# Kernel tuning notes

Hardware: AMD Instinct MI355X
Metric: run time of the kernel (lower is better)

## Reference

```python
import jax, jax.numpy as jnp
import numpy as np

B, T, C, H = 8, 1024, 768, 12
D = C // H  # head dim = 64

def setup_inputs() -> dict:
    key = jax.random.key(0)
    k0, k1, k2, k3, k4 = jax.random.split(key, 5)
    x = jax.random.normal(k0, (B, T, C), dtype=jnp.float32)
    # flax Dense params: kernel [in, out], bias [out]
    c_attn_kernel = jax.random.normal(k1, (C, 3 * C), dtype=jnp.float32) * (1.0 / np.sqrt(C))
    c_attn_bias = jax.random.normal(k2, (3 * C,), dtype=jnp.float32) * 0.01
    c_proj_kernel = jax.random.normal(k3, (C, C), dtype=jnp.float32) * (1.0 / np.sqrt(C))
    c_proj_bias = jax.random.normal(k4, (C,), dtype=jnp.float32) * 0.01
    return {"x": x, "c_attn_kernel": c_attn_kernel, "c_attn_bias": c_attn_bias,
            "c_proj_kernel": c_proj_kernel, "c_proj_bias": c_proj_bias}

def reference(x, c_attn_kernel, c_attn_bias, c_proj_kernel, c_proj_bias):
    Bc, Tc, Cc = x.shape
    qkv = x @ c_attn_kernel + c_attn_bias          # [B, T, 3C]
    q, k, v = jnp.split(qkv, 3, axis=-1)
    q = q.reshape(Bc, Tc, H, D).swapaxes(1, 2)     # [B, H, T, D]
    k = k.reshape(Bc, Tc, H, D).swapaxes(1, 2)
    v = v.reshape(Bc, Tc, H, D).swapaxes(1, 2)
    att = jnp.matmul(q, k.swapaxes(-2, -1)) * (1.0 / jnp.sqrt(jnp.float32(D)))  # [B, H, T, T]
    mask = jnp.tril(jnp.ones((Tc, Tc), dtype=bool)).reshape(1, 1, Tc, Tc)
    att = jnp.where(mask, att, -jnp.inf)
    att = jax.nn.softmax(att, axis=-1)
    # dropout=0.0 / train=False -> identity
    y = jnp.matmul(att, v)                          # [B, H, T, D]
    y = y.swapaxes(1, 2).reshape(Bc, Tc, Cc)        # [B, T, C]
    y = y @ c_proj_kernel + c_proj_bias
    return y
```

## Files before the change

### kernel.cpp

```cpp
#include <hip/hip_runtime.h>
#include <hip/hip_bf16.h>
#include <math.h>

#define BATCH 8
#define SEQ   1024
#define CH    768
#define NH    12
#define HD    64
#define HSZ   (BATCH * NH * SEQ * HD)

typedef __attribute__((ext_vector_type(8))) short short8;
typedef __attribute__((ext_vector_type(4))) short short4v;
typedef __attribute__((ext_vector_type(4))) float floatx4;

static __device__ inline short f2bf(float f) {
    union { float f; unsigned u; } x; x.f = f;
    unsigned r = (x.u + 0x7fffu + ((x.u >> 16) & 1u)) >> 16;
    return (short)r;
}

#define GLOAD_LDS16(g, l)                                                     \
    __builtin_amdgcn_global_load_lds(                                         \
        (const __attribute__((address_space(1))) void*)(g),                   \
        (__attribute__((address_space(3))) void*)(l), 16, 0, 0)

#define NCAST (BATCH * SEQ * CH / 1024)
#define NTA   ((3 * CH / 32) * (CH / 32))
#define NTP   ((CH / 32) * (CH / 32))

__device__ __forceinline__ void transpose_tile(
    const float* __restrict__ w, short* __restrict__ wt, int K, int N,
    int bx, int by, int tid, float (*tile)[33])
{
    const int tx = tid & 31, ty = tid >> 5;
    const int n0 = bx * 32, k0 = by * 32;
    #pragma unroll
    for (int i = 0; i < 4; i++)
        tile[ty + i * 8][tx] = w[(size_t)(k0 + ty + i * 8) * N + n0 + tx];
    __syncthreads();
    #pragma unroll
    for (int i = 0; i < 4; i++)
        wt[(size_t)(n0 + ty + i * 8) * K + k0 + tx] = f2bf(tile[tx][ty + i * 8]);
}

__global__ __launch_bounds__(256) void prep_kernel(
    const float* __restrict__ x, short* __restrict__ xb,
    const float* __restrict__ wa, short* __restrict__ wta,
    const float* __restrict__ wp, short* __restrict__ wtp)
{
    __shared__ float tile[32][33];
    const int bid = blockIdx.x, tid = threadIdx.x;
    if (bid < NCAST) {
        int i = (bid * 256 + tid) * 4;
        float4 v = *(const float4*)(x + i);
        short4v o = { f2bf(v.x), f2bf(v.y), f2bf(v.z), f2bf(v.w) };
        *(short4v*)(xb + i) = o;
    } else if (bid < NCAST + NTA) {
        int t = bid - NCAST;
        transpose_tile(wa, wta, CH, 3 * CH, t % (3 * CH / 32), t / (3 * CH / 32), tid, tile);
    } else {
        int t = bid - NCAST - NTA;
        transpose_tile(wp, wtp, CH, CH, t % (CH / 32), t / (CH / 32), tid, tile);
    }
}

template <int MODE, int BM, int BN, int NBLK, int MBX, int WPE>
__global__ __launch_bounds__(256, WPE) void gemm_bt_kernel(
    const short* __restrict__ A, const short* __restrict__ Bt,
    const float* __restrict__ bias, void* __restrict__ outv,
    int M, int N, int K)
{
    constexpr int MT  = BM / 32;
    constexpr int NT  = BN / 32;
    constexpr int ACH = BM / 64;
    constexpr int BCH = BN / 64;
    constexpr int STAGE_BYTES = (BM + BN) * 128;
    constexpr int EPI_BYTES   = (MODE == 1) ? (BN * 136 * 2) : 0;
    constexpr int LDS_BYTES   = STAGE_BYTES > EPI_BYTES ? STAGE_BYTES : EPI_BYTES;
    __shared__ __align__(16) char smem[LDS_BYTES];
    short* AsB = (short*)smem;
    short* BsB = (short*)(smem + BM * 128);

    const int tid  = threadIdx.x;
    const int lane = tid & 63;
    const int col  = lane & 15;
    const int quad = lane >> 4;
    const int wave = tid >> 6;
    const int wm = wave & 1, wn = wave >> 1;

    const int bid = blockIdx.x;
    const int j   = bid & 7;
    const int t   = bid >> 3;
    const int mb  = j * MBX + t / NBLK;
    const int nb  = t % NBLK;
    const int m0 = mb * BM, n0 = nb * BN;

    const int srow = tid >> 2;
    const int kc   = ((tid & 3) ^ (srow & 3)) * 8;
    const short* aptr[ACH];
    const short* bptr[BCH];
    #pragma unroll
    for (int c = 0; c < ACH; c++)
        aptr[c] = A + (size_t)(m0 + c * 64 + srow) * K + kc;
    #pragma unroll
    for (int c = 0; c < BCH; c++)
        bptr[c] = Bt + (size_t)(n0 + c * 64 + srow) * K + kc;

    floatx4 acc[MT][NT];
    #pragma unroll
    for (int i = 0; i < MT; i++)
        #pragma unroll
        for (int jj = 0; jj < NT; jj++)
            acc[i][jj] = (floatx4){0.f, 0.f, 0.f, 0.f};

    const int niter = K / 32;

    #pragma unroll
    for (int c = 0; c < ACH; c++) GLOAD_LDS16(aptr[c], &AsB[c * 2048 + tid * 8]);
    #pragma unroll
    for (int c = 0; c < BCH; c++) GLOAD_LDS16(bptr[c], &BsB[c * 2048 + tid * 8]);

    for (int k = 0; k < niter; k++) {
        __syncthreads();
        const int cur = k & 1, nxt = cur ^ 1;
        if (k + 1 < niter) {
            const int ko = (k + 1) * 32;
            #pragma unroll
            for (int c = 0; c < ACH; c++)
                GLOAD_LDS16(aptr[c] + ko, &AsB[nxt * BM * 32 + c * 2048 + tid * 8]);
            #pragma unroll
            for (int c = 0; c < BCH; c++)
                GLOAD_LDS16(bptr[c] + ko, &BsB[nxt * BN * 32 + c * 2048 + tid * 8]);
        }
        short8 af[MT], bf[NT];
        #pragma unroll
        for (int mt = 0; mt < MT; mt++) {
            const int row = wm * (BM / 2) + mt * 16 + col;
            af[mt] = *(const short8*)&AsB[cur * BM * 32 + row * 32 + ((quad ^ (row & 3)) << 3)];
        }
        #pragma unroll
        for (int nt = 0; nt < NT; nt++) {
            const int row = wn * (BN / 2) + nt * 16 + col;
            bf[nt] = *(const short8*)&BsB[cur * BN * 32 + row * 32 + ((quad ^ (row & 3)) << 3)];
        }
        #pragma unroll
        for (int mt = 0; mt < MT; mt++)
            #pragma unroll
            for (int nt = 0; nt < NT; nt++)
                acc[mt][nt] = __builtin_amdgcn_mfma_f32_16x16x32_bf16(
                    af[mt], bf[nt], acc[mt][nt], 0, 0, 0);
    }

    if constexpr (MODE == 0) {
        #pragma unroll
        for (int mt = 0; mt < MT; mt++) {
            #pragma unroll
            for (int r = 0; r < 4; r++) {
                const int m = m0 + wm * (BM / 2) + mt * 16 + quad * 4 + r;
                #pragma unroll
                for (int nt = 0; nt < NT; nt++) {
                    const int n = n0 + wn * (BN / 2) + nt * 16 + col;
                    ((float*)outv)[(size_t)m * N + n] = acc[mt][nt][r] + bias[n];
                }
            }
        }
    } else {
        __syncthreads();
        short* Es = (short*)smem;
        const int sel = n0 / CH;
        const int h0  = (n0 - sel * CH) >> 6;
        const int bb  = m0 >> 10;
        const int t0  = m0 & 1023;
        short* qkv = (short*)outv;

        if (sel < 2) {
            #pragma unroll
            for (int mt = 0; mt < MT; mt++)
                #pragma unroll
                for (int r = 0; r < 4; r++) {
                    const int lm = wm * (BM / 2) + mt * 16 + quad * 4 + r;
                    #pragma unroll
                    for (int nt = 0; nt < NT; nt++) {
                        const int ln = wn * (BN / 2) + nt * 16 + col;
                        Es[lm * 200 + ln] = f2bf(acc[mt][nt][r] + bias[n0 + ln]);
                    }
                }
            __syncthreads();
            #pragma unroll
            for (int it = 0; it < (BM * BN / 8) / 256; it++) {
                const int id = it * 256 + tid;
                const int hp = id >> 10, lm = (id >> 3) & 127, dc = id & 7;
                short8 v = *(const short8*)&Es[lm * 200 + hp * 64 + dc * 8];
                size_t dst = (size_t)sel * HSZ +
                    (((size_t)(bb * NH + h0 + hp)) * SEQ + t0 + lm) * HD + dc * 8;
                *(short8*)&qkv[dst] = v;
            }
        } else {
            #pragma unroll
            for (int nt = 0; nt < NT; nt++) {
                const int ln = wn * (BN / 2) + nt * 16 + col;
                const float bv = bias[n0 + ln];
                #pragma unroll
                for (int mt = 0; mt < MT; mt++) {
                    const int lm = wm * (BM / 2) + mt * 16 + quad * 4;
                    short4v pk;
                    #pragma unroll
                    for (int r = 0; r < 4; r++) pk[r] = f2bf(acc[mt][nt][r] + bv);
                    *(short4v*)&Es[ln * 136 + lm] = pk;
                }
            }
            __syncthreads();
            #pragma unroll
            for (int it = 0; it < (BM * BN / 8) / 256; it++) {
                const int id = it * 256 + tid;
                const int ln = id >> 4, tc = id & 15;
                short8 v = *(const short8*)&Es[ln * 136 + tc * 8];
                const int hp = ln >> 6, d = ln & 63;
                size_t dst = (size_t)2 * HSZ +
                    (((size_t)(bb * NH + h0 + hp)) * HD + d) * SEQ + t0 + tc * 8;
                *(short8*)&qkv[dst] = v;
            }
        }
    }
}

#define LDK 72

template <bool DIAG>
__device__ __forceinline__ void strip_step(
    const short* __restrict__ Ksh, const short* __restrict__ Vsh,
    short* __restrict__ pw, const short8* aq, floatx4* acc_o,
    floatx4& lacc, short8 bones, int col, int quad, int qrow0)
{
    floatx4 sacc[4];
    #pragma unroll
    for (int i = 0; i < 4; i++) sacc[i] = (floatx4){0.f, 0.f, 0.f, 0.f};
    #pragma unroll
    for (int s = 0; s < 2; s++)
        #pragma unroll
        for (int nt = 0; nt < 4; nt++) {
            short8 bk = *(const short8*)&Ksh[(nt * 16 + col) * LDK + s * 32 + quad * 8];
            sacc[nt] = __builtin_amdgcn_mfma_f32_16x16x32_bf16(aq[s], bk, sacc[nt], 0, 0, 0);
        }

    const float SCL = 0.18033688011112042f;
    #pragma unroll
    for (int r = 0; r < 4; r++)
        #pragma unroll
        for (int nt = 0; nt < 4; nt++) {
            float sv = sacc[nt][r] * SCL;
            if (DIAG && (nt * 16 + col) > (qrow0 + r)) sv = -INFINITY;
            float pv = __builtin_amdgcn_exp2f(sv);
            pw[(quad * 4 + r) * LDK + nt * 16 + col] =
                (short)(__builtin_bit_cast(unsigned, pv) >> 16);
        }
    __builtin_amdgcn_wave_barrier();

    short8 ap[2];
    ap[0] = *(const short8*)&pw[col * LDK + quad * 8];
    ap[1] = *(const short8*)&pw[col * LDK + 32 + quad * 8];

    #pragma unroll
    for (int s = 0; s < 2; s++) {
        #pragma unroll
        for (int nt = 0; nt < 4; nt++) {
            short8 bv = *(const short8*)&Vsh[(nt * 16 + col) * LDK + s * 32 + quad * 8];
            acc_o[nt] = __builtin_amdgcn_mfma_f32_16x16x32_bf16(ap[s], bv, acc_o[nt], 0, 0, 0);
        }
        lacc = __builtin_amdgcn_mfma_f32_16x16x32_bf16(ap[s], bones, lacc, 0, 0, 0);
    }
}

__global__ __launch_bounds__(256, 3) void attn_kernel(
    const short* __restrict__ Qg, const short* __restrict__ Kg,
    const short* __restrict__ Vg, short* __restrict__ Y)
{
    __shared__ __align__(16) short Ksh[64 * LDK];
    __shared__ __align__(16) short Vsh[64 * LDK];
    __shared__ __align__(16) short Psh[4][2][16 * LDK];

    const int tid  = threadIdx.x;
    const int wave = tid >> 6;
    const int lane = tid & 63;
    const int col  = lane & 15;
    const int quad = lane >> 4;
    const int bid = blockIdx.x;
    const int bh  = bid % 96;
    const int qt  = bid / 96;
    const int b = bh / NH, h = bh - b * NH;

    const size_t kqbase = (size_t)bh * SEQ * HD;
    const size_t vbase  = (size_t)bh * HD * SEQ;

    short8 aq[2][2];
    #pragma unroll
    for (int st = 0; st < 2; st++) {
        const short* qp = Qg + kqbase +
            (size_t)(qt * 128 + st * 64 + wave * 16 + col) * HD + quad * 8;
        aq[st][0] = *(const short8*)(qp);
        aq[st][1] = *(const short8*)(qp + 32);
    }

    floatx4 acc_o[2][4];
    floatx4 lacc[2];
    #pragma unroll
    for (int st = 0; st < 2; st++) {
        lacc[st] = (floatx4){0.f, 0.f, 0.f, 0.f};
        #pragma unroll
        for (int i = 0; i < 4; i++) acc_o[st][i] = (floatx4){0.f, 0.f, 0.f, 0.f};
    }

    const short one_bf = (short)0x3F80;
    short8 bones = (col == 0)
        ? (short8){one_bf, one_bf, one_bf, one_bf, one_bf, one_bf, one_bf, one_bf}
        : (short8){0, 0, 0, 0, 0, 0, 0, 0};

    const int qrow0 = wave * 16 + quad * 4;

    const int idx0 = tid * 8, idx1 = (256 + tid) * 8;
    const int row0 = idx0 >> 6, offs0 = idx0 & 63;
    const int row1 = idx1 >> 6, offs1 = idx1 & 63;

    short8 kreg[2], vreg[2];
    {
        const short* ksrc = Kg + kqbase;
        const short* vsrc = Vg + vbase;
        kreg[0] = *(const short8*)&ksrc[idx0];
        kreg[1] = *(const short8*)&ksrc[idx1];
        vreg[0] = *(const short8*)&vsrc[(size_t)row0 * SEQ + offs0];
        vreg[1] = *(const short8*)&vsrc[(size_t)row1 * SEQ + offs1];
    }

    const int nkt = 2 * qt + 2;
    for (int kt = 0; kt < nkt; kt++) {
        __syncthreads();
        *(short8*)&Ksh[row0 * LDK + offs0] = kreg[0];
        *(short8*)&Ksh[row1 * LDK + offs1] = kreg[1];
        *(short8*)&Vsh[row0 * LDK + offs0] = vreg[0];
        *(short8*)&Vsh[row1 * LDK + offs1] = vreg[1];
        __syncthreads();

        if (kt + 1 < nkt) {
            const short* ksrc = Kg + kqbase + (size_t)(kt + 1) * 64 * HD;
            const short* vsrc = Vg + vbase + (kt + 1) * 64;
            kreg[0] = *(const short8*)&ksrc[idx0];
            kreg[1] = *(const short8*)&ksrc[idx1];
            vreg[0] = *(const short8*)&vsrc[(size_t)row0 * SEQ + offs0];
            vreg[1] = *(const short8*)&vsrc[(size_t)row1 * SEQ + offs1];
        }

        if (kt < 2 * qt) {
            strip_step<false>(Ksh, Vsh, Psh[wave][0], aq[0], acc_o[0], lacc[0],
                              bones, col, quad, qrow0);
            strip_step<false>(Ksh, Vsh, Psh[wave][1], aq[1], acc_o[1], lacc[1],
                              bones, col, quad, qrow0);
        } else if (kt == 2 * qt) {
            strip_step<true>(Ksh, Vsh, Psh[wave][0], aq[0], acc_o[0], lacc[0],
                             bones, col, quad, qrow0);
            strip_step<false>(Ksh, Vsh, Psh[wave][1], aq[1], acc_o[1], lacc[1],
                              bones, col, quad, qrow0);
        } else {
            strip_step<true>(Ksh, Vsh, Psh[wave][1], aq[1], acc_o[1], lacc[1],
                             bones, col, quad, qrow0);
        }
    }

    #pragma unroll
    for (int st = 0; st < 2; st++) {
        #pragma unroll
        for (int r = 0; r < 4; r++) {
            float l = __shfl(lacc[st][r], quad * 16, 64);
            float inv = 1.f / l;
            int t = qt * 128 + st * 64 + wave * 16 + quad * 4 + r;
            size_t ybase = ((size_t)(b * SEQ + t)) * CH + h * HD;
            #pragma unroll
            for (int nt = 0; nt < 4; nt++)
                Y[ybase + nt * 16 + col] = f2bf(acc_o[st][nt][r] * inv);
        }
    }
}

extern "C" void kernel_launch(void* const* d_in, const int* in_sizes, int n_in,
                              void* d_out, int out_size, void* d_ws, size_t ws_size,
                              hipStream_t stream)
{
    const float* x      = (const float*)d_in[0];
    const float* w_attn = (const float*)d_in[1];
    const float* b_attn = (const float*)d_in[2];
    const float* w_proj = (const float*)d_in[3];
    const float* b_proj = (const float*)d_in[4];
    float* out = (float*)d_out;

    short* qkv16 = (short*)d_ws;
    short* y16   = qkv16 + (size_t)3 * HSZ;
    short* xb    = y16   + (size_t)HSZ;
    short* wta   = xb    + (size_t)HSZ;
    short* wtp   = wta   + (size_t)3 * CH * CH;

    const int M = BATCH * SEQ;

    prep_kernel<<<NCAST + NTA + NTP, 256, 0, stream>>>(x, xb, w_attn, wta, w_proj, wtp);

    gemm_bt_kernel<1, 128, 192, 12, 8, 3><<<768, 256, 0, stream>>>(
        xb, wta, b_attn, qkv16, M, 3 * CH, CH);

    attn_kernel<<<768, 256, 0, stream>>>(qkv16, qkv16 + (size_t)HSZ,
                                         qkv16 + (size_t)2 * HSZ, y16);

    gemm_bt_kernel<0, 128, 192, 4, 8, 3><<<256, 256, 0, stream>>>(
        y16, wtp, b_proj, out, M, CH, CH);
}
```

Measured before the change: 175.5 us.

## Split attention query strips across 8 waves and retile output projection GEMM

```diff
diff --git a/kernel.cpp b/kernel.cpp
--- a/kernel.cpp
+++ b/kernel.cpp
@@ -271,13 +271,13 @@
     }
 }
 
-__global__ __launch_bounds__(256, 3) void attn_kernel(
+__global__ __launch_bounds__(512, 4) void attn_kernel(
     const short* __restrict__ Qg, const short* __restrict__ Kg,
     const short* __restrict__ Vg, short* __restrict__ Y)
 {
     __shared__ __align__(16) short Ksh[64 * LDK];
     __shared__ __align__(16) short Vsh[64 * LDK];
-    __shared__ __align__(16) short Psh[4][2][16 * LDK];
+    __shared__ __align__(16) short Psh[8][16 * LDK];
 
     const int tid  = threadIdx.x;
     const int wave = tid >> 6;
@@ -292,91 +292,77 @@
     const size_t kqbase = (size_t)bh * SEQ * HD;
     const size_t vbase  = (size_t)bh * HD * SEQ;
 
-    short8 aq[2][2];
-    #pragma unroll
-    for (int st = 0; st < 2; st++) {
+    short8 aq[2];
+    {
         const short* qp = Qg + kqbase +
-            (size_t)(qt * 128 + st * 64 + wave * 16 + col) * HD + quad * 8;
-        aq[st][0] = *(const short8*)(qp);
-        aq[st][1] = *(const short8*)(qp + 32);
-    }
-
-    floatx4 acc_o[2][4];
-    floatx4 lacc[2];
-    #pragma unroll
-    for (int st = 0; st < 2; st++) {
-        lacc[st] = (floatx4){0.f, 0.f, 0.f, 0.f};
-        #pragma unroll
-        for (int i = 0; i < 4; i++) acc_o[st][i] = (floatx4){0.f, 0.f, 0.f, 0.f};
-    }
+            (size_t)(qt * 128 + wave * 16 + col) * HD + quad * 8;
+        aq[0] = *(const short8*)(qp);
+        aq[1] = *(const short8*)(qp + 32);
+    }
+
+    floatx4 acc_o[4];
+    floatx4 lacc = (floatx4){0.f, 0.f, 0.f, 0.f};
+    #pragma unroll
+    for (int i = 0; i < 4; i++) acc_o[i] = (floatx4){0.f, 0.f, 0.f, 0.f};
 
     const short one_bf = (short)0x3F80;
     short8 bones = (col == 0)
         ? (short8){one_bf, one_bf, one_bf, one_bf, one_bf, one_bf, one_bf, one_bf}
         : (short8){0, 0, 0, 0, 0, 0, 0, 0};
 
-    const int qrow0 = wave * 16 + quad * 4;
-
-    const int idx0 = tid * 8, idx1 = (256 + tid) * 8;
-    const int row0 = idx0 >> 6, offs0 = idx0 & 63;
-    const int row1 = idx1 >> 6, offs1 = idx1 & 63;
-
-    short8 kreg[2], vreg[2];
+    const int qrow0 = (wave & 3) * 16 + quad * 4;
+
+    const int idx = tid * 8;
+    const int row = idx >> 6, offs = idx & 63;
+
+    short8 kreg, vreg;
     {
         const short* ksrc = Kg + kqbase;
         const short* vsrc = Vg + vbase;
-        kreg[0] = *(const short8*)&ksrc[idx0];
-        kreg[1] = *(const short8*)&ksrc[idx1];
-        vreg[0] = *(const short8*)&vsrc[(size_t)row0 * SEQ + offs0];
-        vreg[1] = *(const short8*)&vsrc[(size_t)row1 * SEQ + offs1];
+        kreg = *(const short8*)&ksrc[idx];
+        vreg = *(const short8*)&vsrc[(size_t)row * SEQ + offs];
     }
 
     const int nkt = 2 * qt + 2;
     for (int kt = 0; kt < nkt; kt++) {
         __syncthreads();
-        *(short8*)&Ksh[row0 * LDK + offs0] = kreg[0];
-        *(short8*)&Ksh[row1 * LDK + offs1] = kreg[1];
-        *(short8*)&Vsh[row0 * LDK + offs0] = vreg[0];
-        *(short8*)&Vsh[row1 * LDK + offs1] = vreg[1];
+        *(short8*)&Ksh[row * LDK + offs] = kreg;
+        *(short8*)&Vsh[row * LDK + offs] = vreg;
         __syncthreads();
 
         if (kt + 1 < nkt) {
             const short* ksrc = Kg + kqbase + (size_t)(kt + 1) * 64 * HD;
             const short* vsrc = Vg + vbase + (kt + 1) * 64;
-            kreg[0] = *(const short8*)&ksrc[idx0];
-            kreg[1] = *(const short8*)&ksrc[idx1];
-            vreg[0] = *(const short8*)&vsrc[(size_t)row0 * SEQ + offs0];
-            vreg[1] = *(const short8*)&vsrc[(size_t)row1 * SEQ + offs1];
+            kreg = *(const short8*)&ksrc[idx];
+            vreg = *(const short8*)&vsrc[(size_t)row * SEQ + offs];
         }
 
         if (kt < 2 * qt) {
-            strip_step<false>(Ksh, Vsh, Psh[wave][0], aq[0], acc_o[0], lacc[0],
-                              bones, col, quad, qrow0);
-            strip_step<false>(Ksh, Vsh, Psh[wave][1], aq[1], acc_o[1], lacc[1],
+            strip_step<false>(Ksh, Vsh, Psh[wave], aq, acc_o, lacc,
                               bones, col, quad, qrow0);
         } else if (kt == 2 * qt) {
-            strip_step<true>(Ksh, Vsh, Psh[wave][0], aq[0], acc_o[0], lacc[0],
-                             bones, col, quad, qrow0);
-            strip_step<false>(Ksh, Vsh, Psh[wave][1], aq[1], acc_o[1], lacc[1],
-                              bones, col, quad, qrow0);
+            if (wave < 4)
+                strip_step<true>(Ksh, Vsh, Psh[wave], aq, acc_o, lacc,
+                                 bones, col, quad, qrow0);
+            else
+                strip_step<false>(Ksh, Vsh, Psh[wave], aq, acc_o, lacc,
+                                  bones, col, quad, qrow0);
         } else {
-            strip_step<true>(Ksh, Vsh, Psh[wave][1], aq[1], acc_o[1], lacc[1],
-                             bones, col, quad, qrow0);
-        }
-    }
-
-    #pragma unroll
-    for (int st = 0; st < 2; st++) {
-        #pragma unroll
-        for (int r = 0; r < 4; r++) {
-            float l = __shfl(lacc[st][r], quad * 16, 64);
-            float inv = 1.f / l;
-            int t = qt * 128 + st * 64 + wave * 16 + quad * 4 + r;
-            size_t ybase = ((size_t)(b * SEQ + t)) * CH + h * HD;
-            #pragma unroll
-            for (int nt = 0; nt < 4; nt++)
-                Y[ybase + nt * 16 + col] = f2bf(acc_o[st][nt][r] * inv);
-        }
+            if (wave >= 4)
+                strip_step<true>(Ksh, Vsh, Psh[wave], aq, acc_o, lacc,
+                                 bones, col, quad, qrow0);
+        }
+    }
+
+    #pragma unroll
+    for (int r = 0; r < 4; r++) {
+        float l = __shfl(lacc[r], quad * 16, 64);
+        float inv = 1.f / l;
+        int t = qt * 128 + wave * 16 + quad * 4 + r;
+        size_t ybase = ((size_t)(b * SEQ + t)) * CH + h * HD;
+        #pragma unroll
+        for (int nt = 0; nt < 4; nt++)
+            Y[ybase + nt * 16 + col] = f2bf(acc_o[nt][r] * inv);
     }
 }
 
@@ -404,9 +390,9 @@
     gemm_bt_kernel<1, 128, 192, 12, 8, 3><<<768, 256, 0, stream>>>(
         xb, wta, b_attn, qkv16, M, 3 * CH, CH);
 
-    attn_kernel<<<768, 256, 0, stream>>>(qkv16, qkv16 + (size_t)HSZ,
+    attn_kernel<<<768, 512, 0, stream>>>(qkv16, qkv16 + (size_t)HSZ,
                                          qkv16 + (size_t)2 * HSZ, y16);
 
-    gemm_bt_kernel<0, 128, 192, 4, 8, 3><<<256, 256, 0, stream>>>(
+    gemm_bt_kernel<0, 64, 192, 4, 16, 4><<<512, 256, 0, stream>>>(
         y16, wtp, b_proj, out, M, CH, CH);
 }
```

Result: faster. 171.7 us (-2.2%).
